# Performance work log

Hardware: AMD Instinct MI355X
Metric: run time of the kernel (lower is better)

## Reference

```python
import jax, jax.numpy as jnp
import numpy as np

B, L, H = 2, 256, 256
EXPAND = 2
I = H * EXPAND        # internal_size = 512
S = I                 # state_size must equal internal_size (see broadcast in selective mechanism)
K = 3                 # d_conv (must be odd so 'same' padding holds)
EPS = 1e-5


def _forward(x, W_in, conv_w, conv_b, W_ssm, b_ssm, W_gate, b_gate, A, D, W_out, z, ln_g, ln_b):
    # in_proj: [B,L,H] @ [2I,H]^T -> [B,L,2I] (no bias)
    xp = jnp.einsum('blh,oh->blo', x, W_in)
    x_q, x_k = xp[..., :I], xp[..., I:]
    # conv1d over time, full channel mixing (I -> I), 'same' padding, with bias
    xk = jnp.transpose(x_k, (0, 2, 1))  # [B,I,L]
    xk = jax.lax.conv_general_dilated(xk, conv_w, (1,), [((K - 1) // 2, (K - 1) // 2)],
                                      dimension_numbers=('NCH', 'OIH', 'NCH'))
    xk = xk + conv_b[None, :, None]
    x_k = jnp.transpose(xk, (0, 2, 1))  # [B,L,I]
    x_q = jax.nn.gelu(x_q, approximate=False)  # torch F.gelu default = exact erf
    xc = x_q + x_k  # x_combined [B,L,I]

    # selective mechanism
    ssm = jnp.einsum('bli,oi->blo', xc, W_ssm) + b_ssm      # [B,L,2S+I]
    gate = jax.nn.sigmoid(jnp.einsum('bli,oi->blo', xc, W_gate) + b_gate)  # [B,L,S+I]
    C_w = ssm[..., S:2 * S]          # [B,L,S]
    D_w = ssm[..., 2 * S:]           # [B,L,I]
    C_weight = gate[..., S:] * C_w   # requires S == I
    D_weight = D_w * D_w

    x_out = xc * D_weight            # [B,L,I]
    u = x_out[..., :S]               # state input [B,L,S]

    # recurrence: h_0 = u_0 (broadcast over I); h_t = h_{t-1} * A + u_t (broadcast over I)
    # (init h = 0 reproduces the i==0 branch: 0*A + u_0)
    def step(h, u_t):
        h = h * A + u_t[:, :, None]  # [B,S,I]
        return h, h

    h0 = jnp.zeros((B, S, I), x_out.dtype)
    _, hs = jax.lax.scan(step, h0, jnp.transpose(u, (1, 0, 2)))  # hs: [L,B,S,I]

    C_applied = jnp.einsum('lbsi,bls->bli', hs, C_weight)  # [B,L,I]
    y = C_applied + x_out * D
    out = jnp.einsum('bli,hi->blh', y, W_out)  # out_proj, no bias

    # LayerNorm over last dim
    mu = jnp.mean(out, axis=-1, keepdims=True)
    var = jnp.mean(jnp.square(out - mu), axis=-1, keepdims=True)
    out = (out - mu) * jax.lax.rsqrt(var + EPS) * ln_g + ln_b

    out = out * z  # z is shape (1,)
    return out + x


def setup_inputs() -> dict:
    key = jax.random.key(0)
    ks = jax.random.split(key, 10)
    n = lambda k, shape, s: jax.random.normal(k, shape, jnp.float32) * s
    return {
        'x': n(ks[0], (B, L, H), 1.0),
        'W_in': n(ks[1], (2 * I, H), 1.0 / np.sqrt(H)),
        'conv_w': n(ks[2], (I, I, K), 1.0 / np.sqrt(I * K)),
        'conv_b': n(ks[3], (I,), 0.02),
        'W_ssm': n(ks[4], (2 * S + I, I), 1.0 / np.sqrt(I)),
        'b_ssm': n(ks[5], (2 * S + I,), 0.02),
        'W_gate': n(ks[6], (S + I, I), 1.0 / np.sqrt(I)),
        'b_gate': n(ks[7], (S + I,), 0.02),
        'A': jax.random.uniform(ks[8], (S, I), jnp.float32, 0.0, 0.95),  # keep recurrence stable
        'D': jnp.ones((I,), jnp.float32),
        'W_out': n(ks[9], (H, I), 1.0 / np.sqrt(I)),
        'z': jnp.ones((1,), jnp.float32),
        'ln_g': jnp.ones((H,), jnp.float32),
        'ln_b': jnp.zeros((H,), jnp.float32),
    }


def reference(x, W_in, conv_w, conv_b, W_ssm, b_ssm, W_gate, b_gate, A, D, W_out, z, ln_g, ln_b):
    return _forward(x, W_in, conv_w, conv_b, W_ssm, b_ssm, W_gate, b_gate, A, D, W_out, z, ln_g, ln_b)
```

## Files before the change

### kernel.cpp

```cpp
#include <hip/hip_runtime.h>
#include <math.h>

#define NB    2
#define LSEQ  256
#define HDIM  256
#define IDIM  512
#define NROW  512
#define NC    8
#define TCH   32

typedef __attribute__((ext_vector_type(8))) short bf16x8;
typedef __attribute__((ext_vector_type(4))) float f32x4;

__device__ inline unsigned short f2b(float f) {
    unsigned u = __float_as_uint(f);
    return (unsigned short)((u + 0x7FFFu + ((u >> 16) & 1u)) >> 16);
}

__global__ __launch_bounds__(256) void kcvt(const float* __restrict__ x,
                                            const float* __restrict__ W_in,
                                            const float* __restrict__ conv_w,
                                            const float* __restrict__ W_ssm,
                                            const float* __restrict__ W_gate,
                                            const float* __restrict__ b_ssm,
                                            const float* __restrict__ b_gate,
                                            const float* __restrict__ W_out,
                                            unsigned short* __restrict__ xb,
                                            unsigned short* __restrict__ Wb,
                                            unsigned short* __restrict__ cwb,
                                            unsigned short* __restrict__ Wsgb,
                                            float* __restrict__ bsg,
                                            unsigned short* __restrict__ W_outb) {
    const int stride = gridDim.x * 256;
    const int t0 = blockIdx.x * 256 + threadIdx.x;
    for (int i = t0; i < 131072; i += stride) xb[i] = f2b(x[i]);
    for (int i = t0; i < 262144; i += stride) Wb[i] = f2b(W_in[i]);
    for (int d = t0; d < 262144; d += stride) {
        const float* s = conv_w + (size_t)d * 3;
        cwb[d]          = f2b(s[0]);
        cwb[262144 + d] = f2b(s[1]);
        cwb[524288 + d] = f2b(s[2]);
    }
    for (int d = t0; d < 786432; d += stride) {
        int j = d >> 9, i = d & 511;
        float v = (j < 1024) ? W_ssm[(size_t)(512 + j) * 512 + i]
                             : W_gate[(size_t)(j - 512) * 512 + i];
        Wsgb[d] = f2b(v);
    }
    for (int j = t0; j < 1536; j += stride)
        bsg[j] = (j < 1024) ? b_ssm[512 + j] : b_gate[j - 512];
    for (int i = t0; i < 131072; i += stride) W_outb[i] = f2b(W_out[i]);
}

__global__ __launch_bounds__(256) void k1_mfma(const unsigned short* __restrict__ xb,
                                               const unsigned short* __restrict__ Wb,
                                               float* __restrict__ xq_g,
                                               unsigned short* __restrict__ xkb) {
    const int t = threadIdx.x;
    const int w = blockIdx.x * 4 + (t >> 6);
    const int lane = t & 63;
    const int mt = w >> 6, nt = w & 63;
    const int r0 = mt * 16, n0 = nt * 16;
    const int fr = lane & 15, fk = (lane >> 4) * 8;
    const unsigned short* ap = xb + (size_t)(r0 + fr) * HDIM + fk;
    const unsigned short* bp = Wb + (size_t)(n0 + fr) * HDIM + fk;
    f32x4 acc = {0.f, 0.f, 0.f, 0.f};
    #pragma unroll
    for (int k0 = 0; k0 < HDIM; k0 += 32) {
        bf16x8 av = *(const bf16x8*)(ap + k0);
        bf16x8 bv = *(const bf16x8*)(bp + k0);
        acc = __builtin_amdgcn_mfma_f32_16x16x32_bf16(av, bv, acc, 0, 0, 0);
    }
    const int orow = (lane >> 4) * 4;
    const int oc = n0 + fr;
    if (oc < IDIM) {
        #pragma unroll
        for (int j = 0; j < 4; ++j) {
            float v = acc[j];
            xq_g[(size_t)(r0 + orow + j) * IDIM + oc] =
                0.5f * v * (1.0f + erff(v * 0.70710678118654752f));
        }
    } else {
        #pragma unroll
        for (int j = 0; j < 4; ++j)
            xkb[(size_t)(r0 + orow + j) * IDIM + (oc - IDIM)] = f2b(acc[j]);
    }
}

__global__ __launch_bounds__(256) void kxc_mfma(const unsigned short* __restrict__ xkb,
                                                const unsigned short* __restrict__ cwb,
                                                const float* __restrict__ xq_g,
                                                const float* __restrict__ conv_b,
                                                float* __restrict__ xc,
                                                unsigned short* __restrict__ xcb) {
    const int t = threadIdx.x;
    const int w = blockIdx.x * 4 + (t >> 6);
    const int lane = t & 63;
    const int mt = w >> 5, nt = w & 31;
    const int r0 = mt * 16, o0 = nt * 16;
    const int fr = lane & 15, fk = (lane >> 4) * 8;
    const int g = r0 + fr;
    const int lo = r0 & ~255, hi = lo + 256;
    const bool okm = (g - 1 >= lo), okp = (g + 1 < hi);
    const unsigned short* am = xkb + (size_t)(g - 1) * IDIM + fk;
    const unsigned short* a0 = xkb + (size_t)g * IDIM + fk;
    const unsigned short* ap = xkb + (size_t)(g + 1) * IDIM + fk;
    const unsigned short* b0 = cwb + (size_t)(o0 + fr) * IDIM + fk;
    const unsigned short* b1 = b0 + 262144;
    const unsigned short* b2 = b0 + 524288;
    const bf16x8 zz = {0, 0, 0, 0, 0, 0, 0, 0};
    f32x4 acc = {0.f, 0.f, 0.f, 0.f};
    #pragma unroll
    for (int k0 = 0; k0 < IDIM; k0 += 32) {
        bf16x8 avm = okm ? *(const bf16x8*)(am + k0) : zz;
        bf16x8 av0 = *(const bf16x8*)(a0 + k0);
        bf16x8 avp = okp ? *(const bf16x8*)(ap + k0) : zz;
        bf16x8 bv0 = *(const bf16x8*)(b0 + k0);
        bf16x8 bv1 = *(const bf16x8*)(b1 + k0);
        bf16x8 bv2 = *(const bf16x8*)(b2 + k0);
        acc = __builtin_amdgcn_mfma_f32_16x16x32_bf16(avm, bv0, acc, 0, 0, 0);
        acc = __builtin_amdgcn_mfma_f32_16x16x32_bf16(av0, bv1, acc, 0, 0, 0);
        acc = __builtin_amdgcn_mfma_f32_16x16x32_bf16(avp, bv2, acc, 0, 0, 0);
    }
    const int orow = (lane >> 4) * 4;
    const int oc = o0 + fr;
    const float cb = conv_b[oc];
    #pragma unroll
    for (int j = 0; j < 4; ++j) {
        int r = r0 + orow + j;
        float v = acc[j] + xq_g[(size_t)r * IDIM + oc] + cb;
        xc[(size_t)r * IDIM + oc] = v;
        xcb[(size_t)r * IDIM + oc] = f2b(v);
    }
}

__global__ __launch_bounds__(256) void k3f_mfma(const unsigned short* __restrict__ xcb,
                                                const unsigned short* __restrict__ Wsgb,
                                                const float* __restrict__ bsg,
                                                const float* __restrict__ xc,
                                                float* __restrict__ Cw,
                                                float* __restrict__ u) {
    const int t = threadIdx.x;
    const int w = blockIdx.x * 4 + (t >> 6);
    const int lane = t & 63;
    const int mt = w >> 5, nt = w & 31;
    const int r0 = mt * 16, s0 = nt * 16;
    const int fr = lane & 15, fk = (lane >> 4) * 8;
    const unsigned short* ap = xcb + (size_t)(r0 + fr) * IDIM + fk;
    const unsigned short* b0 = Wsgb + (size_t)(s0 + fr) * IDIM + fk;
    const unsigned short* b1 = Wsgb + (size_t)(512 + s0 + fr) * IDIM + fk;
    const unsigned short* b2 = Wsgb + (size_t)(1024 + s0 + fr) * IDIM + fk;
    f32x4 ac0 = {0.f, 0.f, 0.f, 0.f};
    f32x4 ac1 = {0.f, 0.f, 0.f, 0.f};
    f32x4 ac2 = {0.f, 0.f, 0.f, 0.f};
    #pragma unroll
    for (int k0 = 0; k0 < IDIM; k0 += 32) {
        bf16x8 av  = *(const bf16x8*)(ap + k0);
        bf16x8 bv0 = *(const bf16x8*)(b0 + k0);
        bf16x8 bv1 = *(const bf16x8*)(b1 + k0);
        bf16x8 bv2 = *(const bf16x8*)(b2 + k0);
        ac0 = __builtin_amdgcn_mfma_f32_16x16x32_bf16(av, bv0, ac0, 0, 0, 0);
        ac1 = __builtin_amdgcn_mfma_f32_16x16x32_bf16(av, bv1, ac1, 0, 0, 0);
        ac2 = __builtin_amdgcn_mfma_f32_16x16x32_bf16(av, bv2, ac2, 0, 0, 0);
    }
    const int orow = (lane >> 4) * 4;
    const int sc = s0 + fr;
    const float bc = bsg[sc], bd = bsg[512 + sc], bg = bsg[1024 + sc];
    #pragma unroll
    for (int j = 0; j < 4; ++j) {
        int r = r0 + orow + j;
        float craw = ac0[j] + bc;
        float dw   = ac1[j] + bd;
        float graw = ac2[j] + bg;
        float gv = 1.0f / (1.0f + expf(-graw));
        float xcv = xc[(size_t)r * IDIM + sc];
        Cw[(size_t)r * IDIM + sc] = gv * craw;
        u[(size_t)r * IDIM + sc]  = xcv * dw * dw;
    }
}

__global__ __launch_bounds__(256) void k4a_pass1(const float* __restrict__ u,
                                                 const float* __restrict__ A,
                                                 float* __restrict__ C_loc) {
    const int wave = (blockIdx.x * 256 + threadIdx.x) >> 6;
    const int lane = threadIdx.x & 63;
    const int ig = wave & 63;
    const int c  = (wave >> 6) & (NC - 1);
    const int b  = wave >> 9;
    const int i8 = ig * 8;
    const int s8 = lane * 8;
    float a[8][8], h[8][8];
    #pragma unroll
    for (int j = 0; j < 8; ++j) {
        float4 a0 = *(const float4*)&A[(size_t)(s8 + j) * IDIM + i8];
        float4 a1 = *(const float4*)&A[(size_t)(s8 + j) * IDIM + i8 + 4];
        a[j][0] = a0.x; a[j][1] = a0.y; a[j][2] = a0.z; a[j][3] = a0.w;
        a[j][4] = a1.x; a[j][5] = a1.y; a[j][6] = a1.z; a[j][7] = a1.w;
        #pragma unroll
        for (int ii = 0; ii < 8; ++ii) h[j][ii] = 0.f;
    }
    const float* ub = u + ((size_t)b * LSEQ + c * TCH) * IDIM;
    for (int l = 0; l < TCH; ++l) {
        float4 u0 = *(const float4*)(ub + l * IDIM + s8);
        float4 u1 = *(const float4*)(ub + l * IDIM + s8 + 4);
        float uu[8] = {u0.x, u0.y, u0.z, u0.w, u1.x, u1.y, u1.z, u1.w};
        #pragma unroll
        for (int ii = 0; ii < 8; ++ii)
            #pragma unroll
            for (int j = 0; j < 8; ++j)
                h[j][ii] = h[j][ii] * a[j][ii] + uu[j];
    }
    #pragma unroll
    for (int ii = 0; ii < 8; ++ii) {
        float* cp = C_loc + (((size_t)b * NC + c) * IDIM + i8 + ii) * IDIM + s8;
        float4 v0, v1;
        v0.x = h[0][ii]; v0.y = h[1][ii]; v0.z = h[2][ii]; v0.w = h[3][ii];
        v1.x = h[4][ii]; v1.y = h[5][ii]; v1.z = h[6][ii]; v1.w = h[7][ii];
        *(float4*)cp = v0;
        *(float4*)(cp + 4) = v1;
    }
}

__global__ __launch_bounds__(256) void k4b_combine(const float* __restrict__ A,
                                                   float* __restrict__ C_loc) {
    int idx = blockIdx.x * 256 + threadIdx.x;
    int s4 = (idx & 127) * 4;
    int i  = (idx >> 7) & 511;
    int b  = idx >> 16;
    float da[4], h4[4] = {0.0f, 0.0f, 0.0f, 0.0f};
    #pragma unroll
    for (int j = 0; j < 4; ++j) {
        float aa = A[(size_t)(s4 + j) * IDIM + i];
        aa = aa * aa; aa = aa * aa; aa = aa * aa;
        aa = aa * aa; aa = aa * aa;
        da[j] = aa;
    }
    for (int c = 0; c < NC; ++c) {
        size_t base = (((size_t)b * NC + c) * IDIM + i) * IDIM + s4;
        float4 cl = *(const float4*)&C_loc[base];
        float4 hv;
        hv.x = h4[0]; hv.y = h4[1]; hv.z = h4[2]; hv.w = h4[3];
        *(float4*)&C_loc[base] = hv;
        h4[0] = h4[0] * da[0] + cl.x;
        h4[1] = h4[1] * da[1] + cl.y;
        h4[2] = h4[2] * da[2] + cl.z;
        h4[3] = h4[3] * da[3] + cl.w;
    }
}

__global__ __launch_bounds__(256) void k4c_pass2(const float* __restrict__ u,
                                                 const float* __restrict__ Cw,
                                                 const float* __restrict__ A,
                                                 const float* __restrict__ D,
                                                 const float* __restrict__ H,
                                                 unsigned short* __restrict__ ybb) {
    const int wave = (blockIdx.x * 256 + threadIdx.x) >> 6;
    const int lane = threadIdx.x & 63;
    const int ig = wave & 63;
    const int c  = (wave >> 6) & (NC - 1);
    const int b  = wave >> 9;
    const int i8 = ig * 8;
    const int s8 = lane * 8;
    float a[8][8], h[8][8];
    #pragma unroll
    for (int j = 0; j < 8; ++j) {
        float4 a0 = *(const float4*)&A[(size_t)(s8 + j) * IDIM + i8];
        float4 a1 = *(const float4*)&A[(size_t)(s8 + j) * IDIM + i8 + 4];
        a[j][0] = a0.x; a[j][1] = a0.y; a[j][2] = a0.z; a[j][3] = a0.w;
        a[j][4] = a1.x; a[j][5] = a1.y; a[j][6] = a1.z; a[j][7] = a1.w;
    }
    #pragma unroll
    for (int ii = 0; ii < 8; ++ii) {
        const float* hp = H + (((size_t)b * NC + c) * IDIM + i8 + ii) * IDIM + s8;
        float4 h0v = *(const float4*)hp;
        float4 h1v = *(const float4*)(hp + 4);
        h[0][ii] = h0v.x; h[1][ii] = h0v.y; h[2][ii] = h0v.z; h[3][ii] = h0v.w;
        h[4][ii] = h1v.x; h[5][ii] = h1v.y; h[6][ii] = h1v.z; h[7][ii] = h1v.w;
    }
    float4 D0 = *(const float4*)&D[i8];
    float4 D1 = *(const float4*)&D[i8 + 4];
    const float Di[8] = {D0.x, D0.y, D0.z, D0.w, D1.x, D1.y, D1.z, D1.w};
    const float* ub = u + (size_t)b * LSEQ * IDIM;
    const float* cb = Cw + (size_t)b * LSEQ * IDIM;
    unsigned short* yb = ybb + (size_t)b * LSEQ * IDIM;
    for (int l0 = c * TCH; l0 < c * TCH + TCH; l0 += 2) {
        float p[2][8];
        #pragma unroll
        for (int j = 0; j < 2; ++j) {
            const int l = l0 + j;
            float4 u0 = *(const float4*)(ub + l * IDIM + s8);
            float4 u1 = *(const float4*)(ub + l * IDIM + s8 + 4);
            float4 c0 = *(const float4*)(cb + l * IDIM + s8);
            float4 c1 = *(const float4*)(cb + l * IDIM + s8 + 4);
            float uu[8] = {u0.x, u0.y, u0.z, u0.w, u1.x, u1.y, u1.z, u1.w};
            float cc[8] = {c0.x, c0.y, c0.z, c0.w, c1.x, c1.y, c1.z, c1.w};
            #pragma unroll
            for (int ii = 0; ii < 8; ++ii) {
                float acc = 0.f;
                #pragma unroll
                for (int k = 0; k < 8; ++k) {
                    h[k][ii] = h[k][ii] * a[k][ii] + uu[k];
                    acc += cc[k] * h[k][ii];
                }
                p[j][ii] = acc;
            }
        }
        #pragma unroll
        for (int off = 1; off < 64; off <<= 1) {
            #pragma unroll
            for (int j = 0; j < 2; ++j)
                #pragma unroll
                for (int ii = 0; ii < 8; ++ii)
                    p[j][ii] += __shfl_xor(p[j][ii], off, 64);
        }
        if (lane == 0) {
            #pragma unroll
            for (int j = 0; j < 2; ++j) {
                float4 ul0 = *(const float4*)&ub[(size_t)(l0 + j) * IDIM + i8];
                float4 ul1 = *(const float4*)&ub[(size_t)(l0 + j) * IDIM + i8 + 4];
                const float ul[8] = {ul0.x, ul0.y, ul0.z, ul0.w,
                                     ul1.x, ul1.y, ul1.z, ul1.w};
                #pragma unroll
                for (int ii = 0; ii < 8; ++ii)
                    yb[(size_t)(l0 + j) * IDIM + i8 + ii] = f2b(p[j][ii] + ul[ii] * Di[ii]);
            }
        }
    }
}

__global__ __launch_bounds__(256) void k5a_mfma(const unsigned short* __restrict__ ybb,
                                                const unsigned short* __restrict__ W_outb,
                                                float* __restrict__ outlin) {
    const int t = threadIdx.x;
    const int w = blockIdx.x * 4 + (t >> 6);
    const int lane = t & 63;
    const int mt = w >> 4, nt = w & 15;
    const int r0 = mt * 16, h0 = nt * 16;
    const int fr = lane & 15, fk = (lane >> 4) * 8;
    const unsigned short* ap = ybb + (size_t)(r0 + fr) * IDIM + fk;
    const unsigned short* bp = W_outb + (size_t)(h0 + fr) * IDIM + fk;
    f32x4 acc = {0.f, 0.f, 0.f, 0.f};
    #pragma unroll
    for (int k0 = 0; k0 < IDIM; k0 += 32) {
        bf16x8 av = *(const bf16x8*)(ap + k0);
        bf16x8 bv = *(const bf16x8*)(bp + k0);
        acc = __builtin_amdgcn_mfma_f32_16x16x32_bf16(av, bv, acc, 0, 0, 0);
    }
    const int orow = (lane >> 4) * 4;
    const int hc = h0 + fr;
    #pragma unroll
    for (int j = 0; j < 4; ++j)
        outlin[(size_t)(r0 + orow + j) * HDIM + hc] = acc[j];
}

__global__ __launch_bounds__(256) void k5b_ln(const float* __restrict__ outlin,
                                              const float* __restrict__ x,
                                              const float* __restrict__ z,
                                              const float* __restrict__ ln_g,
                                              const float* __restrict__ ln_b,
                                              float* __restrict__ out) {
    const int r = blockIdx.x;
    const int t = threadIdx.x;
    float v = outlin[(size_t)r * HDIM + t];
    float s1 = v, s2 = v * v;
    #pragma unroll
    for (int off = 1; off < 64; off <<= 1) {
        s1 += __shfl_xor(s1, off, 64);
        s2 += __shfl_xor(s2, off, 64);
    }
    __shared__ float r1[4], r2[4];
    const int w = t >> 6, lane = t & 63;
    if (lane == 0) { r1[w] = s1; r2[w] = s2; }
    __syncthreads();
    float t1 = r1[0] + r1[1] + r1[2] + r1[3];
    float t2 = r2[0] + r2[1] + r2[2] + r2[3];
    float mu = t1 * (1.0f / 256.0f);
    float var = t2 * (1.0f / 256.0f) - mu * mu;
    float inv = rsqrtf(var + 1e-5f);
    float o = (v - mu) * inv * ln_g[t] + ln_b[t];
    out[(size_t)r * HDIM + t] = o * z[0] + x[(size_t)r * HDIM + t];
}

extern "C" void kernel_launch(void* const* d_in, const int* in_sizes, int n_in,
                              void* d_out, int out_size, void* d_ws, size_t ws_size,
                              hipStream_t stream) {
    const float* x      = (const float*)d_in[0];
    const float* W_in   = (const float*)d_in[1];
    const float* conv_w = (const float*)d_in[2];
    const float* conv_b = (const float*)d_in[3];
    const float* W_ssm  = (const float*)d_in[4];
    const float* b_ssm  = (const float*)d_in[5];
    const float* W_gate = (const float*)d_in[6];
    const float* b_gate = (const float*)d_in[7];
    const float* A      = (const float*)d_in[8];
    const float* D      = (const float*)d_in[9];
    const float* W_out  = (const float*)d_in[10];
    const float* z      = (const float*)d_in[11];
    const float* ln_g   = (const float*)d_in[12];
    const float* ln_b   = (const float*)d_in[13];
    float* out = (float*)d_out;

    float* ws = (float*)d_ws;
    float*          xq_g   = ws;
    float*          xc     = ws + 262144;
    float*          Cw     = ws + 524288;
    float*          u      = ws + 786432;
    float*          outlin = ws + 1048576;
    float*          bsg    = ws + 1179648;
    unsigned short* xcb    = (unsigned short*)(ws + 1181696);
    unsigned short* xkb    = (unsigned short*)(ws + 1312768);
    unsigned short* Wsgb   = (unsigned short*)(ws + 1443840);
    unsigned short* W_outb = (unsigned short*)(ws + 1837056);
    unsigned short* ybb    = (unsigned short*)(ws + 1902592);
    float*          area   = ws + 2033664;
    unsigned short* xb     = (unsigned short*)area;
    unsigned short* Wb     = (unsigned short*)(area + 65536);
    unsigned short* cwb    = (unsigned short*)(area + 196608);
    float*          C_loc  = area;

    kcvt       <<<512, 256, 0, stream>>>(x, W_in, conv_w, W_ssm, W_gate, b_ssm,
                                         b_gate, W_out, xb, Wb, cwb, Wsgb, bsg, W_outb);
    k1_mfma    <<<512, 256, 0, stream>>>(xb, Wb, xq_g, xkb);
    kxc_mfma   <<<256, 256, 0, stream>>>(xkb, cwb, xq_g, conv_b, xc, xcb);
    k3f_mfma   <<<256, 256, 0, stream>>>(xcb, Wsgb, bsg, xc, Cw, u);
    k4a_pass1  <<<256, 256, 0, stream>>>(u, A, C_loc);
    k4b_combine<<<512, 256, 0, stream>>>(A, C_loc);
    k4c_pass2  <<<256, 256, 0, stream>>>(u, Cw, A, D, C_loc, ybb);
    k5a_mfma   <<<128, 256, 0, stream>>>(ybb, W_outb, outlin);
    k5b_ln     <<<512, 256, 0, stream>>>(outlin, x, z, ln_g, ln_b, out);
}
```

Baseline: 103.2 us.

## Fuse chunked scan passes into one cooperative kernel with split state dimension

Merges the three chunked-scan kernels (local pass, chunk combine, output pass) into a single cooperative launch that separates phases with grid-wide syncs. Each wave now handles half the state dimension with 4 states per lane instead of 8, so the grid doubles to 512 blocks and register pressure per thread drops. The cross-lane reduction becomes a transpose-style shuffle that writes partial sums per state half, and a final phase adds the two halves and the D skip term. This trades launch overhead for grid-sync cost and an extra partial-sum round trip through memory (reusing the xq workspace region).

```diff
diff --git a/kernel.cpp b/kernel.cpp
--- a/kernel.cpp
+++ b/kernel.cpp
@@ -1,4 +1,5 @@
 #include <hip/hip_runtime.h>
+#include <hip/hip_cooperative_groups.h>
 #include <math.h>
 
 #define NB    2
@@ -179,152 +180,138 @@
     }
 }
 
-__global__ __launch_bounds__(256) void k4a_pass1(const float* __restrict__ u,
-                                                 const float* __restrict__ A,
-                                                 float* __restrict__ C_loc) {
-    const int wave = (blockIdx.x * 256 + threadIdx.x) >> 6;
+__global__ __launch_bounds__(256, 2) void k4_fused(const float* __restrict__ u,
+                                                   const float* __restrict__ Cw,
+                                                   const float* __restrict__ A,
+                                                   const float* __restrict__ D,
+                                                   float* __restrict__ C_loc,
+                                                   float* __restrict__ patl,
+                                                   unsigned short* __restrict__ ybb) {
+    cooperative_groups::grid_group grid = cooperative_groups::this_grid();
+    const int tid = blockIdx.x * 256 + threadIdx.x;
+    const int wave = tid >> 6;
     const int lane = threadIdx.x & 63;
     const int ig = wave & 63;
-    const int c  = (wave >> 6) & (NC - 1);
-    const int b  = wave >> 9;
+    const int sh = (wave >> 6) & 1;
+    const int c  = (wave >> 7) & (NC - 1);
+    const int b  = wave >> 10;
     const int i8 = ig * 8;
-    const int s8 = lane * 8;
-    float a[8][8], h[8][8];
-    #pragma unroll
-    for (int j = 0; j < 8; ++j) {
-        float4 a0 = *(const float4*)&A[(size_t)(s8 + j) * IDIM + i8];
-        float4 a1 = *(const float4*)&A[(size_t)(s8 + j) * IDIM + i8 + 4];
-        a[j][0] = a0.x; a[j][1] = a0.y; a[j][2] = a0.z; a[j][3] = a0.w;
-        a[j][4] = a1.x; a[j][5] = a1.y; a[j][6] = a1.z; a[j][7] = a1.w;
-        #pragma unroll
-        for (int ii = 0; ii < 8; ++ii) h[j][ii] = 0.f;
-    }
-    const float* ub = u + ((size_t)b * LSEQ + c * TCH) * IDIM;
-    for (int l = 0; l < TCH; ++l) {
-        float4 u0 = *(const float4*)(ub + l * IDIM + s8);
-        float4 u1 = *(const float4*)(ub + l * IDIM + s8 + 4);
-        float uu[8] = {u0.x, u0.y, u0.z, u0.w, u1.x, u1.y, u1.z, u1.w};
-        #pragma unroll
-        for (int ii = 0; ii < 8; ++ii)
+    const int s4 = sh * 256 + lane * 4;
+
+    float a[4][8], h[4][8];
+    #pragma unroll
+    for (int k = 0; k < 4; ++k) {
+        float4 a0 = *(const float4*)&A[(size_t)(s4 + k) * IDIM + i8];
+        float4 a1 = *(const float4*)&A[(size_t)(s4 + k) * IDIM + i8 + 4];
+        a[k][0] = a0.x; a[k][1] = a0.y; a[k][2] = a0.z; a[k][3] = a0.w;
+        a[k][4] = a1.x; a[k][5] = a1.y; a[k][6] = a1.z; a[k][7] = a1.w;
+        #pragma unroll
+        for (int ii = 0; ii < 8; ++ii) h[k][ii] = 0.f;
+    }
+
+    {
+        const float* ub = u + ((size_t)b * LSEQ + c * TCH) * IDIM;
+        for (int l = 0; l < TCH; ++l) {
+            float4 u4 = *(const float4*)(ub + l * IDIM + s4);
+            float uu[4] = {u4.x, u4.y, u4.z, u4.w};
             #pragma unroll
-            for (int j = 0; j < 8; ++j)
-                h[j][ii] = h[j][ii] * a[j][ii] + uu[j];
-    }
-    #pragma unroll
-    for (int ii = 0; ii < 8; ++ii) {
-        float* cp = C_loc + (((size_t)b * NC + c) * IDIM + i8 + ii) * IDIM + s8;
-        float4 v0, v1;
-        v0.x = h[0][ii]; v0.y = h[1][ii]; v0.z = h[2][ii]; v0.w = h[3][ii];
-        v1.x = h[4][ii]; v1.y = h[5][ii]; v1.z = h[6][ii]; v1.w = h[7][ii];
-        *(float4*)cp = v0;
-        *(float4*)(cp + 4) = v1;
-    }
-}
-
-__global__ __launch_bounds__(256) void k4b_combine(const float* __restrict__ A,
-                                                   float* __restrict__ C_loc) {
-    int idx = blockIdx.x * 256 + threadIdx.x;
-    int s4 = (idx & 127) * 4;
-    int i  = (idx >> 7) & 511;
-    int b  = idx >> 16;
-    float da[4], h4[4] = {0.0f, 0.0f, 0.0f, 0.0f};
-    #pragma unroll
-    for (int j = 0; j < 4; ++j) {
-        float aa = A[(size_t)(s4 + j) * IDIM + i];
-        aa = aa * aa; aa = aa * aa; aa = aa * aa;
-        aa = aa * aa; aa = aa * aa;
-        da[j] = aa;
-    }
-    for (int c = 0; c < NC; ++c) {
-        size_t base = (((size_t)b * NC + c) * IDIM + i) * IDIM + s4;
-        float4 cl = *(const float4*)&C_loc[base];
-        float4 hv;
-        hv.x = h4[0]; hv.y = h4[1]; hv.z = h4[2]; hv.w = h4[3];
-        *(float4*)&C_loc[base] = hv;
-        h4[0] = h4[0] * da[0] + cl.x;
-        h4[1] = h4[1] * da[1] + cl.y;
-        h4[2] = h4[2] * da[2] + cl.z;
-        h4[3] = h4[3] * da[3] + cl.w;
-    }
-}
-
-__global__ __launch_bounds__(256) void k4c_pass2(const float* __restrict__ u,
-                                                 const float* __restrict__ Cw,
-                                                 const float* __restrict__ A,
-                                                 const float* __restrict__ D,
-                                                 const float* __restrict__ H,
-                                                 unsigned short* __restrict__ ybb) {
-    const int wave = (blockIdx.x * 256 + threadIdx.x) >> 6;
-    const int lane = threadIdx.x & 63;
-    const int ig = wave & 63;
-    const int c  = (wave >> 6) & (NC - 1);
-    const int b  = wave >> 9;
-    const int i8 = ig * 8;
-    const int s8 = lane * 8;
-    float a[8][8], h[8][8];
-    #pragma unroll
-    for (int j = 0; j < 8; ++j) {
-        float4 a0 = *(const float4*)&A[(size_t)(s8 + j) * IDIM + i8];
-        float4 a1 = *(const float4*)&A[(size_t)(s8 + j) * IDIM + i8 + 4];
-        a[j][0] = a0.x; a[j][1] = a0.y; a[j][2] = a0.z; a[j][3] = a0.w;
-        a[j][4] = a1.x; a[j][5] = a1.y; a[j][6] = a1.z; a[j][7] = a1.w;
-    }
-    #pragma unroll
-    for (int ii = 0; ii < 8; ++ii) {
-        const float* hp = H + (((size_t)b * NC + c) * IDIM + i8 + ii) * IDIM + s8;
-        float4 h0v = *(const float4*)hp;
-        float4 h1v = *(const float4*)(hp + 4);
-        h[0][ii] = h0v.x; h[1][ii] = h0v.y; h[2][ii] = h0v.z; h[3][ii] = h0v.w;
-        h[4][ii] = h1v.x; h[5][ii] = h1v.y; h[6][ii] = h1v.z; h[7][ii] = h1v.w;
-    }
-    float4 D0 = *(const float4*)&D[i8];
-    float4 D1 = *(const float4*)&D[i8 + 4];
-    const float Di[8] = {D0.x, D0.y, D0.z, D0.w, D1.x, D1.y, D1.z, D1.w};
-    const float* ub = u + (size_t)b * LSEQ * IDIM;
-    const float* cb = Cw + (size_t)b * LSEQ * IDIM;
-    unsigned short* yb = ybb + (size_t)b * LSEQ * IDIM;
-    for (int l0 = c * TCH; l0 < c * TCH + TCH; l0 += 2) {
-        float p[2][8];
-        #pragma unroll
-        for (int j = 0; j < 2; ++j) {
-            const int l = l0 + j;
-            float4 u0 = *(const float4*)(ub + l * IDIM + s8);
-            float4 u1 = *(const float4*)(ub + l * IDIM + s8 + 4);
-            float4 c0 = *(const float4*)(cb + l * IDIM + s8);
-            float4 c1 = *(const float4*)(cb + l * IDIM + s8 + 4);
-            float uu[8] = {u0.x, u0.y, u0.z, u0.w, u1.x, u1.y, u1.z, u1.w};
-            float cc[8] = {c0.x, c0.y, c0.z, c0.w, c1.x, c1.y, c1.z, c1.w};
+            for (int ii = 0; ii < 8; ++ii)
+                #pragma unroll
+                for (int k = 0; k < 4; ++k)
+                    h[k][ii] = h[k][ii] * a[k][ii] + uu[k];
+        }
+        #pragma unroll
+        for (int ii = 0; ii < 8; ++ii) {
+            float4 v;
+            v.x = h[0][ii]; v.y = h[1][ii]; v.z = h[2][ii]; v.w = h[3][ii];
+            *(float4*)&C_loc[(((size_t)b * NC + c) * IDIM + i8 + ii) * IDIM + s4] = v;
+        }
+    }
+    grid.sync();
+
+    {
+        const int ss4 = (tid & 127) * 4;
+        const int i  = (tid >> 7) & 511;
+        const int bb = tid >> 16;
+        float da[4], h4[4] = {0.f, 0.f, 0.f, 0.f};
+        #pragma unroll
+        for (int j = 0; j < 4; ++j) {
+            float aa = A[(size_t)(ss4 + j) * IDIM + i];
+            aa = aa * aa; aa = aa * aa; aa = aa * aa;
+            aa = aa * aa; aa = aa * aa;
+            da[j] = aa;
+        }
+        for (int cc = 0; cc < NC; ++cc) {
+            size_t base = (((size_t)bb * NC + cc) * IDIM + i) * IDIM + ss4;
+            float4 cl = *(const float4*)&C_loc[base];
+            float4 hv;
+            hv.x = h4[0]; hv.y = h4[1]; hv.z = h4[2]; hv.w = h4[3];
+            *(float4*)&C_loc[base] = hv;
+            h4[0] = h4[0] * da[0] + cl.x;
+            h4[1] = h4[1] * da[1] + cl.y;
+            h4[2] = h4[2] * da[2] + cl.z;
+            h4[3] = h4[3] * da[3] + cl.w;
+        }
+    }
+    grid.sync();
+
+    {
+        #pragma unroll
+        for (int ii = 0; ii < 8; ++ii) {
+            float4 hv = *(const float4*)&C_loc[(((size_t)b * NC + c) * IDIM + i8 + ii) * IDIM + s4];
+            h[0][ii] = hv.x; h[1][ii] = hv.y; h[2][ii] = hv.z; h[3][ii] = hv.w;
+        }
+        const float* ub = u + (size_t)b * LSEQ * IDIM;
+        const float* cb = Cw + (size_t)b * LSEQ * IDIM;
+        float* prow = patl + ((size_t)(b * 2 + sh) * LSEQ) * IDIM;
+        const bool w8 = ((lane & 7) == 0);
+        const int iiw = lane >> 3;
+        for (int l = c * TCH; l < c * TCH + TCH; ++l) {
+            float4 u4 = *(const float4*)(ub + l * IDIM + s4);
+            float4 c4 = *(const float4*)(cb + l * IDIM + s4);
+            float uu[4] = {u4.x, u4.y, u4.z, u4.w};
+            float cc[4] = {c4.x, c4.y, c4.z, c4.w};
+            float p[8];
             #pragma unroll
             for (int ii = 0; ii < 8; ++ii) {
                 float acc = 0.f;
                 #pragma unroll
-                for (int k = 0; k < 8; ++k) {
+                for (int k = 0; k < 4; ++k) {
                     h[k][ii] = h[k][ii] * a[k][ii] + uu[k];
                     acc += cc[k] * h[k][ii];
                 }
-                p[j][ii] = acc;
+                p[ii] = acc;
             }
-        }
-        #pragma unroll
-        for (int off = 1; off < 64; off <<= 1) {
             #pragma unroll
-            for (int j = 0; j < 2; ++j)
-                #pragma unroll
-                for (int ii = 0; ii < 8; ++ii)
-                    p[j][ii] += __shfl_xor(p[j][ii], off, 64);
-        }
-        if (lane == 0) {
+            for (int ii = 0; ii < 8; ++ii) p[ii] += __shfl_xor(p[ii], 8, 64);
             #pragma unroll
-            for (int j = 0; j < 2; ++j) {
-                float4 ul0 = *(const float4*)&ub[(size_t)(l0 + j) * IDIM + i8];
-                float4 ul1 = *(const float4*)&ub[(size_t)(l0 + j) * IDIM + i8 + 4];
-                const float ul[8] = {ul0.x, ul0.y, ul0.z, ul0.w,
-                                     ul1.x, ul1.y, ul1.z, ul1.w};
-                #pragma unroll
-                for (int ii = 0; ii < 8; ++ii)
-                    yb[(size_t)(l0 + j) * IDIM + i8 + ii] = f2b(p[j][ii] + ul[ii] * Di[ii]);
-            }
-        }
+            for (int ii = 0; ii < 8; ++ii) p[ii] += __shfl_xor(p[ii], 16, 64);
+            #pragma unroll
+            for (int ii = 0; ii < 8; ++ii) p[ii] += __shfl_xor(p[ii], 32, 64);
+            float q = (lane & 32) ? ((lane & 16) ? ((lane & 8) ? p[7] : p[6])
+                                                 : ((lane & 8) ? p[5] : p[4]))
+                                  : ((lane & 16) ? ((lane & 8) ? p[3] : p[2])
+                                                 : ((lane & 8) ? p[1] : p[0]));
+            q += __shfl_xor(q, 1, 64);
+            q += __shfl_xor(q, 2, 64);
+            q += __shfl_xor(q, 4, 64);
+            if (w8) prow[(size_t)l * IDIM + i8 + iiw] = q;
+        }
+    }
+    grid.sync();
+
+    {
+        const int idx = tid * 2;
+        const int i = idx & 511;
+        const int l = (idx >> 9) & 255;
+        const int bb = idx >> 17;
+        float2 p0 = *(const float2*)&patl[(((size_t)bb * 2 + 0) * LSEQ + l) * IDIM + i];
+        float2 p1 = *(const float2*)&patl[(((size_t)bb * 2 + 1) * LSEQ + l) * IDIM + i];
+        float2 uv = *(const float2*)&u[((size_t)bb * LSEQ + l) * IDIM + i];
+        float2 dv = *(const float2*)&D[i];
+        size_t yo = ((size_t)bb * LSEQ + l) * IDIM + i;
+        ybb[yo]     = f2b(p0.x + p1.x + uv.x * dv.x);
+        ybb[yo + 1] = f2b(p0.y + p1.y + uv.y * dv.y);
     }
 }
 
@@ -403,6 +390,7 @@
     float* ws = (float*)d_ws;
     float*          xq_g   = ws;
     float*          xc     = ws + 262144;
+    float*          patl   = ws;
     float*          Cw     = ws + 524288;
     float*          u      = ws + 786432;
     float*          outlin = ws + 1048576;
@@ -418,14 +406,23 @@
     unsigned short* cwb    = (unsigned short*)(area + 196608);
     float*          C_loc  = area;
 
-    kcvt       <<<512, 256, 0, stream>>>(x, W_in, conv_w, W_ssm, W_gate, b_ssm,
-                                         b_gate, W_out, xb, Wb, cwb, Wsgb, bsg, W_outb);
-    k1_mfma    <<<512, 256, 0, stream>>>(xb, Wb, xq_g, xkb);
-    kxc_mfma   <<<256, 256, 0, stream>>>(xkb, cwb, xq_g, conv_b, xc, xcb);
-    k3f_mfma   <<<256, 256, 0, stream>>>(xcb, Wsgb, bsg, xc, Cw, u);
-    k4a_pass1  <<<256, 256, 0, stream>>>(u, A, C_loc);
-    k4b_combine<<<512, 256, 0, stream>>>(A, C_loc);
-    k4c_pass2  <<<256, 256, 0, stream>>>(u, Cw, A, D, C_loc, ybb);
-    k5a_mfma   <<<128, 256, 0, stream>>>(ybb, W_outb, outlin);
-    k5b_ln     <<<512, 256, 0, stream>>>(outlin, x, z, ln_g, ln_b, out);
-}
+    kcvt     <<<512, 256, 0, stream>>>(x, W_in, conv_w, W_ssm, W_gate, b_ssm,
+                                       b_gate, W_out, xb, Wb, cwb, Wsgb, bsg, W_outb);
+    k1_mfma  <<<512, 256, 0, stream>>>(xb, Wb, xq_g, xkb);
+    kxc_mfma <<<256, 256, 0, stream>>>(xkb, cwb, xq_g, conv_b, xc, xcb);
+    k3f_mfma <<<256, 256, 0, stream>>>(xcb, Wsgb, bsg, xc, Cw, u);
+
+    {
+        const float* u_c = u;  const float* Cw_c = Cw;
+        const float* A_c = A;  const float* D_c = D;
+        float* C_loc_c = C_loc; float* patl_c = patl;
+        unsigned short* ybb_c = ybb;
+        void* args[] = {(void*)&u_c, (void*)&Cw_c, (void*)&A_c, (void*)&D_c,
+                        (void*)&C_loc_c, (void*)&patl_c, (void*)&ybb_c};
+        hipLaunchCooperativeKernel((void*)k4_fused, dim3(512), dim3(256),
+                                   args, 0, stream);
+    }
+
+    k5a_mfma <<<128, 256, 0, stream>>>(ybb, W_outb, outlin);
+    k5b_ln   <<<512, 256, 0, stream>>>(outlin, x, z, ln_g, ln_b, out);
+}
```

Measured after the change: 284.9 us. +176.1%, slower.
